# Performance work log

Hardware: AMD Instinct MI355X
Metric: run time of the kernel (lower is better)

The kernel has to match this reference:

```python
import jax, jax.numpy as jnp
import numpy as np

VOCAB = 50000
EMB = 128
RADIUS = 3
REGION = 2 * RADIUS + 1
BATCH, SEQ = 32, 1024


def setup_inputs() -> dict:
    key = jax.random.key(0)
    k1, k2, k3 = jax.random.split(key, 3)
    seq = jax.random.randint(k1, (BATCH, SEQ), 0, VOCAB, dtype=jnp.int32)
    W = jax.random.normal(k2, (VOCAB - 1, EMB), dtype=jnp.float32) * 0.05
    U = jax.random.normal(k3, ((VOCAB - 1) * REGION, EMB), dtype=jnp.float32) * 0.05
    return {"seq": seq, "W": W, "U": U}


def reference(seq, W, U):
    # pad token id 0 maps to zero rows prepended to W and U
    W_full = jnp.concatenate([jnp.zeros((1, EMB), W.dtype), W], axis=0)          # [V, E]
    U_full = jnp.concatenate([jnp.zeros((REGION, EMB), U.dtype), U], axis=0)     # [V*R, E]

    padded = jnp.pad(seq, ((0, 0), (RADIUS, RADIUS)))                            # [B, S+2r]
    # window indices: pos + offset for offset in [0, REGION)
    idx = jnp.arange(SEQ)[:, None] + jnp.arange(REGION)[None, :]                 # [S, R]
    windows = padded[:, idx]                                                     # [B, S, R]
    align_idx = windows * REGION + jnp.arange(REGION)                            # [B, S, R]

    trigram_emb = W_full[seq]                                                    # [B, S, E]
    align_emb = U_full[align_idx]                                                # [B, S, R, E]

    projected = align_emb * trigram_emb[:, :, None, :]                           # [B, S, R, E]
    h = jnp.max(projected, axis=2)                                               # [B, S, E]
    return h
```

## Files before the change

kernel.cpp:

```cpp
#include <hip/hip_runtime.h>
#include <math.h>

constexpr int kVocab  = 50000;
constexpr int kEmb    = 128;
constexpr int kRegion = 7;
constexpr int kRadius = 3;
constexpr int kBatch  = 32;
constexpr int kSeq    = 1024;
constexpr int kPos    = kBatch * kSeq;
constexpr int kPosPerBlock = 8;

__global__ __launch_bounds__(256) void region_encoder_kernel(
    const int*   __restrict__ seq,
    const float* __restrict__ W,
    const float* __restrict__ U,
    float*       __restrict__ out)
{
    const int lane     = threadIdx.x & 31;
    const int posLocal = threadIdx.x >> 5;
    const int pos      = blockIdx.x * kPosPerBlock + posLocal;
    const int b        = pos >> 10;
    const int s        = pos & (kSeq - 1);

    const int t = seq[pos];
    float4 wv = make_float4(0.f, 0.f, 0.f, 0.f);
    if (t > 0) {
        wv = ((const float4*)(W + (size_t)(t - 1) * kEmb))[lane];
    }

    int wt[kRegion];
#pragma unroll
    for (int r = 0; r < kRegion; ++r) {
        const int sp = s + r - kRadius;
        wt[r] = (sp >= 0 && sp < kSeq) ? seq[b * kSeq + sp] : 0;
    }

    float4 uv[kRegion];
#pragma unroll
    for (int r = 0; r < kRegion; ++r) {
        if (wt[r] > 0) {
            const size_t row = (size_t)(wt[r] - 1) * kRegion + r;
            uv[r] = ((const float4*)(U + row * kEmb))[lane];
        } else {
            uv[r] = make_float4(0.f, 0.f, 0.f, 0.f);
        }
    }

    float4 m;
    m.x = uv[0].x * wv.x;
    m.y = uv[0].y * wv.y;
    m.z = uv[0].z * wv.z;
    m.w = uv[0].w * wv.w;
#pragma unroll
    for (int r = 1; r < kRegion; ++r) {
        m.x = fmaxf(m.x, uv[r].x * wv.x);
        m.y = fmaxf(m.y, uv[r].y * wv.y);
        m.z = fmaxf(m.z, uv[r].z * wv.z);
        m.w = fmaxf(m.w, uv[r].w * wv.w);
    }

    ((float4*)out)[(size_t)pos * (kEmb / 4) + lane] = m;
}

extern "C" void kernel_launch(void* const* d_in, const int* in_sizes, int n_in,
                              void* d_out, int out_size, void* d_ws, size_t ws_size,
                              hipStream_t stream) {
    const int*   seq = (const int*)d_in[0];
    const float* W   = (const float*)d_in[1];
    const float* U   = (const float*)d_in[2];
    float*       out = (float*)d_out;

    const int blocks = kPos / kPosPerBlock;
    region_encoder_kernel<<<dim3(blocks), dim3(256), 0, stream>>>(seq, W, U, out);
}
```

Baseline: 251.1 us.

## Stage contiguous per-token U blocks in LDS per sequence tile

Each block now handles a tile of 16 positions. For every token in the tile plus its radius halo, it loads that token's full 7-row U block (contiguous) into shared memory, then reads the diagonal rows from LDS for each position's max-product. This replaces scattered 512-byte row gathers with contiguous 3.5KB block reads that are shared across neighbouring positions. The cost is extra halo traffic (22 tokens loaded per 16 outputs), about 79KB of LDS per block, low occupancy, and a load phase that is not overlapped with compute because of the barrier.

```diff
diff --git a/kernel.cpp b/kernel.cpp
--- a/kernel.cpp
+++ b/kernel.cpp
@@ -1,65 +1,74 @@
 #include <hip/hip_runtime.h>
 #include <math.h>
 
-constexpr int kVocab  = 50000;
 constexpr int kEmb    = 128;
 constexpr int kRegion = 7;
 constexpr int kRadius = 3;
 constexpr int kBatch  = 32;
 constexpr int kSeq    = 1024;
-constexpr int kPos    = kBatch * kSeq;
-constexpr int kPosPerBlock = 8;
 
-__global__ __launch_bounds__(256) void region_encoder_kernel(
+constexpr int T  = 16;
+constexpr int NT = T + 2 * kRadius;
+constexpr int kBlockFloats = kRegion * kEmb;
+constexpr int kQuads  = kBlockFloats / 4;
+constexpr int kStride = kBlockFloats + 4;
+
+__global__ __launch_bounds__(256, 2) void region_encoder_kernel(
     const int*   __restrict__ seq,
     const float* __restrict__ W,
     const float* __restrict__ U,
     float*       __restrict__ out)
 {
-    const int lane     = threadIdx.x & 31;
-    const int posLocal = threadIdx.x >> 5;
-    const int pos      = blockIdx.x * kPosPerBlock + posLocal;
-    const int b        = pos >> 10;
-    const int s        = pos & (kSeq - 1);
+    __shared__ float lds[NT * kStride];
 
-    const int t = seq[pos];
-    float4 wv = make_float4(0.f, 0.f, 0.f, 0.f);
-    if (t > 0) {
-        wv = ((const float4*)(W + (size_t)(t - 1) * kEmb))[lane];
+    const int tile = blockIdx.x;
+    const int b    = tile >> 6;
+    const int s0   = (tile & 63) * T;
+
+    for (int k = threadIdx.x; k < NT * kQuads; k += 256) {
+        const int j = k / kQuads;
+        const int q = k - j * kQuads;
+        const int p = s0 - kRadius + j;
+        int t = 0;
+        if (p >= 0 && p < kSeq) t = seq[b * kSeq + p];
+        float4 v = make_float4(0.f, 0.f, 0.f, 0.f);
+        if (t > 0) {
+            v = ((const float4*)(U + (size_t)(t - 1) * kBlockFloats))[q];
+        }
+        *(float4*)&lds[j * kStride + q * 4] = v;
     }
+    __syncthreads();
 
-    int wt[kRegion];
+    const int lane = threadIdx.x & 31;
+    const int grp  = threadIdx.x >> 5;
+
+    for (int i = grp; i < T; i += 8) {
+        const int s   = s0 + i;
+        const int pos = b * kSeq + s;
+
+        const int t = seq[pos];
+        float4 wv = make_float4(0.f, 0.f, 0.f, 0.f);
+        if (t > 0) {
+            wv = ((const float4*)(W + (size_t)(t - 1) * kEmb))[lane];
+        }
+
+        float4 u0 = *(const float4*)&lds[(i + 0) * kStride + 0 * kEmb + lane * 4];
+        float4 m;
+        m.x = u0.x * wv.x;
+        m.y = u0.y * wv.y;
+        m.z = u0.z * wv.z;
+        m.w = u0.w * wv.w;
 #pragma unroll
-    for (int r = 0; r < kRegion; ++r) {
-        const int sp = s + r - kRadius;
-        wt[r] = (sp >= 0 && sp < kSeq) ? seq[b * kSeq + sp] : 0;
+        for (int r = 1; r < kRegion; ++r) {
+            float4 u = *(const float4*)&lds[(i + r) * kStride + r * kEmb + lane * 4];
+            m.x = fmaxf(m.x, u.x * wv.x);
+            m.y = fmaxf(m.y, u.y * wv.y);
+            m.z = fmaxf(m.z, u.z * wv.z);
+            m.w = fmaxf(m.w, u.w * wv.w);
+        }
+
+        ((float4*)out)[(size_t)pos * (kEmb / 4) + lane] = m;
     }
-
-    float4 uv[kRegion];
-#pragma unroll
-    for (int r = 0; r < kRegion; ++r) {
-        if (wt[r] > 0) {
-            const size_t row = (size_t)(wt[r] - 1) * kRegion + r;
-            uv[r] = ((const float4*)(U + row * kEmb))[lane];
-        } else {
-            uv[r] = make_float4(0.f, 0.f, 0.f, 0.f);
-        }
-    }
-
-    float4 m;
-    m.x = uv[0].x * wv.x;
-    m.y = uv[0].y * wv.y;
-    m.z = uv[0].z * wv.z;
-    m.w = uv[0].w * wv.w;
-#pragma unroll
-    for (int r = 1; r < kRegion; ++r) {
-        m.x = fmaxf(m.x, uv[r].x * wv.x);
-        m.y = fmaxf(m.y, uv[r].y * wv.y);
-        m.z = fmaxf(m.z, uv[r].z * wv.z);
-        m.w = fmaxf(m.w, uv[r].w * wv.w);
-    }
-
-    ((float4*)out)[(size_t)pos * (kEmb / 4) + lane] = m;
 }
 
 extern "C" void kernel_launch(void* const* d_in, const int* in_sizes, int n_in,
@@ -70,6 +79,6 @@
     const float* U   = (const float*)d_in[2];
     float*       out = (float*)d_out;
 
-    const int blocks = kPos / kPosPerBlock;
+    const int blocks = kBatch * (kSeq / T);
     region_encoder_kernel<<<dim3(blocks), dim3(256), 0, stream>>>(seq, W, U, out);
 }
```

Result: slower. 309.7 us (+23.3%).

## Pair adjacent positions per wavefront and share contiguous U gathers via shuffles

Applied to the files above, without the earlier changes.

Each 64-lane wavefront now handles two adjacent sequence positions. For a token shared by both windows, the two U rows it needs (region offsets j-1 and j) sit next to each other in memory, so a single 64-lane float4 load fetches both. The halves then swap data with a cross-half __shfl so each position gets the row it needs, and only the two edge tokens need a separate 32-lane load. This cuts the number of gather instructions and makes each gather a wider contiguous access, at the cost of 24 shuffles per thread and more register pressure.

```diff
diff --git a/kernel.cpp b/kernel.cpp
--- a/kernel.cpp
+++ b/kernel.cpp
@@ -1,14 +1,12 @@
 #include <hip/hip_runtime.h>
 #include <math.h>
 
-constexpr int kVocab  = 50000;
 constexpr int kEmb    = 128;
 constexpr int kRegion = 7;
 constexpr int kRadius = 3;
 constexpr int kBatch  = 32;
 constexpr int kSeq    = 1024;
 constexpr int kPos    = kBatch * kSeq;
-constexpr int kPosPerBlock = 8;
 
 __global__ __launch_bounds__(256) void region_encoder_kernel(
     const int*   __restrict__ seq,
@@ -16,50 +14,73 @@
     const float* __restrict__ U,
     float*       __restrict__ out)
 {
-    const int lane     = threadIdx.x & 31;
-    const int posLocal = threadIdx.x >> 5;
-    const int pos      = blockIdx.x * kPosPerBlock + posLocal;
-    const int b        = pos >> 10;
-    const int s        = pos & (kSeq - 1);
+    const int lane64 = threadIdx.x & 63;
+    const int half   = lane64 >> 5;
+    const int lane32 = lane64 & 31;
+    const int wid    = threadIdx.x >> 6;
+    const int pairE  = blockIdx.x * 4 + wid;
+    const int b      = pairE >> 9;
+    const int sE     = (pairE & 511) * 2;
+    const int s      = sE + half;
+    const int pos    = b * kSeq + s;
 
-    const int t = seq[pos];
-    float4 wv = make_float4(0.f, 0.f, 0.f, 0.f);
-    if (t > 0) {
-        wv = ((const float4*)(W + (size_t)(t - 1) * kEmb))[lane];
+    int tok[8];
+#pragma unroll
+    for (int j = 0; j < 8; ++j) {
+        const int p = sE - 3 + j;
+        tok[j] = (p >= 0 && p < kSeq) ? seq[b * kSeq + p] : 0;
     }
 
-    int wt[kRegion];
-#pragma unroll
-    for (int r = 0; r < kRegion; ++r) {
-        const int sp = s + r - kRadius;
-        wt[r] = (sp >= 0 && sp < kSeq) ? seq[b * kSeq + sp] : 0;
+    const int t = tok[3 + half];
+    float4 wv = make_float4(0.f, 0.f, 0.f, 0.f);
+    if (t > 0) wv = ((const float4*)(W + (size_t)(t - 1) * kEmb))[lane32];
+
+    const int tE = half ? tok[7] : tok[0];
+    float4 uEdge = make_float4(0.f, 0.f, 0.f, 0.f);
+    if (tE > 0) {
+        const size_t q = (size_t)(tE - 1) * (kRegion * kEmb / 4)
+                       + (half ? 6 * (kEmb / 4) : 0) + lane32;
+        uEdge = ((const float4*)U)[q];
     }
 
-    float4 uv[kRegion];
+    float4 uIn[6];
 #pragma unroll
-    for (int r = 0; r < kRegion; ++r) {
-        if (wt[r] > 0) {
-            const size_t row = (size_t)(wt[r] - 1) * kRegion + r;
-            uv[r] = ((const float4*)(U + row * kEmb))[lane];
-        } else {
-            uv[r] = make_float4(0.f, 0.f, 0.f, 0.f);
+    for (int j = 1; j <= 6; ++j) {
+        const int tp = tok[j];
+        float4 v = make_float4(0.f, 0.f, 0.f, 0.f);
+        if (tp > 0) {
+            const size_t q = (size_t)(tp - 1) * (kRegion * kEmb / 4)
+                           + (size_t)(j - 1) * (kEmb / 4) + lane64;
+            v = ((const float4*)U)[q];
         }
+        uIn[j - 1] = v;
+    }
+
+    const int src = lane64 ^ 32;
+#pragma unroll
+    for (int j = 0; j < 6; ++j) {
+        float4 v = uIn[j];
+        v.x = __shfl(v.x, src, 64);
+        v.y = __shfl(v.y, src, 64);
+        v.z = __shfl(v.z, src, 64);
+        v.w = __shfl(v.w, src, 64);
+        uIn[j] = v;
     }
 
     float4 m;
-    m.x = uv[0].x * wv.x;
-    m.y = uv[0].y * wv.y;
-    m.z = uv[0].z * wv.z;
-    m.w = uv[0].w * wv.w;
+    m.x = uEdge.x * wv.x;
+    m.y = uEdge.y * wv.y;
+    m.z = uEdge.z * wv.z;
+    m.w = uEdge.w * wv.w;
 #pragma unroll
-    for (int r = 1; r < kRegion; ++r) {
-        m.x = fmaxf(m.x, uv[r].x * wv.x);
-        m.y = fmaxf(m.y, uv[r].y * wv.y);
-        m.z = fmaxf(m.z, uv[r].z * wv.z);
-        m.w = fmaxf(m.w, uv[r].w * wv.w);
+    for (int j = 0; j < 6; ++j) {
+        m.x = fmaxf(m.x, uIn[j].x * wv.x);
+        m.y = fmaxf(m.y, uIn[j].y * wv.y);
+        m.z = fmaxf(m.z, uIn[j].z * wv.z);
+        m.w = fmaxf(m.w, uIn[j].w * wv.w);
     }
 
-    ((float4*)out)[(size_t)pos * (kEmb / 4) + lane] = m;
+    ((float4*)out)[(size_t)pos * (kEmb / 4) + lane32] = m;
 }
 
 extern "C" void kernel_launch(void* const* d_in, const int* in_sizes, int n_in,
@@ -70,6 +91,6 @@
     const float* U   = (const float*)d_in[2];
     float*       out = (float*)d_out;
 
-    const int blocks = kPos / kPosPerBlock;
+    const int blocks = kPos / 8;
     region_encoder_kernel<<<dim3(blocks), dim3(256), 0, stream>>>(seq, W, U, out);
 }
```

New measurement: 252.3 us. No clear change (+0.5%).
